# Optimization experiments

Measured on AMD Instinct MI355X. Metric: run time of the kernel, lower is better.

Reference implementation:

```python
import jax, jax.numpy as jnp
import numpy as np

HIDDEN = 128
N_HID = 7            # hidden_layers - 1 internal GELU blocks
N_TERMS = 2          # number of separable terms per side
N_IN = 1             # vars per term
B = 16384
STEP_SIZE = 0.1
NUM_STEPS = 1

# Forest-Ruth 4th-order symplectic coefficients
_K = 2.0 ** (1.0 / 3.0)
_C = (1.0 / (2.0 * (2.0 - _K)), (1.0 - _K) / (2.0 * (2.0 - _K)),
      (1.0 - _K) / (2.0 * (2.0 - _K)), 1.0 / (2.0 * (2.0 - _K)))
_D = (1.0 / (2.0 - _K), -_K / (2.0 - _K), 1.0 / (2.0 - _K), 0.0)


def _mlp(W0, b0, Wh, bh, Wo, bo, x):
    # x: [B, n_in] -> [B, 1]; torch GELU default is exact (erf)
    h = jax.nn.gelu(x @ W0 + b0, approximate=False)
    for i in range(N_HID):
        h = jax.nn.gelu(h @ Wh[i] + bh[i], approximate=False)
    return h @ Wo + bo


def _side_scalar(W0, b0, Wh, bh, Wo, bo, idx, x):
    # gather per-term feature subsets, run all term-MLPs batched via vmap,
    # sum over terms and batch (GradientWrapper takes grad of the summed scalar)
    xs = jnp.moveaxis(x[:, idx], 1, 0)            # [n_terms, B, n_in]
    outs = jax.vmap(_mlp)(W0, b0, Wh, bh, Wo, bo, xs)  # [n_terms, B, 1]
    return outs.sum()


def setup_inputs() -> dict:
    key = jax.random.key(0)
    ks = jax.random.split(key, 3)
    s = 0.05

    def pset(k):
        kk = jax.random.split(k, 6)
        return (
            jax.random.normal(kk[0], (N_TERMS, N_IN, HIDDEN), jnp.float32) * s,
            jax.random.normal(kk[1], (N_TERMS, HIDDEN), jnp.float32) * s,
            jax.random.normal(kk[2], (N_TERMS, N_HID, HIDDEN, HIDDEN), jnp.float32) * s,
            jax.random.normal(kk[3], (N_TERMS, N_HID, HIDDEN), jnp.float32) * s,
            jax.random.normal(kk[4], (N_TERMS, HIDDEN, 1), jnp.float32) * s,
            jax.random.normal(kk[5], (N_TERMS, 1), jnp.float32) * s,
        )

    lW0, lb0, lWh, lbh, lWo, lbo = pset(ks[0])
    rW0, rb0, rWh, rbh, rWo, rbo = pset(ks[1])
    X = jax.random.normal(ks[2], (B, 4), jnp.float32)
    left_idx = jnp.arange(N_TERMS, dtype=jnp.int32).reshape(N_TERMS, N_IN)
    right_idx = jnp.arange(N_TERMS, dtype=jnp.int32).reshape(N_TERMS, N_IN)
    return dict(X=X, lW0=lW0, lb0=lb0, lWh=lWh, lbh=lbh, lWo=lWo, lbo=lbo,
                rW0=rW0, rb0=rb0, rWh=rWh, rbh=rbh, rWo=rWo, rbo=rbo,
                left_idx=left_idx, right_idx=right_idx)


def reference(X, lW0, lb0, lWh, lbh, lWo, lbo,
              rW0, rb0, rWh, rbh, rWo, rbo, left_idx, right_idx):
    # H(q, p) = V(q) + T(p); left side = V(q), right side = T(p)
    dVdq = jax.grad(lambda q: _side_scalar(lW0, lb0, lWh, lbh, lWo, lbo, left_idx, q))
    dTdp = jax.grad(lambda p: _side_scalar(rW0, rb0, rWh, rbh, rWo, rbo, right_idx, p))
    dt = jnp.float32(STEP_SIZE)
    nq = X.shape[1] // 2
    q = X[:, :nq]
    p = X[:, nq:]
    for _ in range(NUM_STEPS):
        for c, d in zip(_C, _D):
            q = q + jnp.float32(c) * dt * dTdp(p)   # dq/dt =  dH/dp
            p = p - jnp.float32(d) * dt * dVdq(q)   # dp/dt = -dH/dq
    return jnp.concatenate((q, p), axis=1)
```

## Files before the change

### kernel.cpp

```cpp
#include <hip/hip_runtime.h>

#define NLAYER 7
#define IMGB 16384
#define WSCALE 16.0f

typedef __attribute__((ext_vector_type(2))) float float2v;
typedef __attribute__((ext_vector_type(4))) float float4v;
typedef __attribute__((ext_vector_type(4))) unsigned int uint4v;
typedef __attribute__((ext_vector_type(4))) int int4v;
typedef __attribute__((ext_vector_type(8))) int int8v;
typedef unsigned long long u64;

__device__ __forceinline__ float2v pk_fma(float2v a, float2v b, float2v c){
  return __builtin_elementwise_fma(a, b, c);
}
__device__ __forceinline__ float2v lo2(float4v v){ return (float2v){v[0], v[1]}; }
__device__ __forceinline__ float2v hi2(float4v v){ return (float2v){v[2], v[3]}; }

__device__ __forceinline__ unsigned pk4fp8(float v0, float v1, float v2, float v3){
  int w = __builtin_amdgcn_cvt_pk_fp8_f32(v0, v1, 0, false);
  w = __builtin_amdgcn_cvt_pk_fp8_f32(v2, v3, w, true);
  return (unsigned)w;
}
template<bool HI>
__device__ __forceinline__ float2v up2(unsigned w){
  return __builtin_amdgcn_cvt_pk_f32_fp8((int)w, HI);
}
__device__ __forceinline__ float4v mfma128s(int8v a, int8v b, unsigned sc){
  return __builtin_amdgcn_mfma_scale_f32_16x16x128_f8f6f4(
      a, b, (float4v){0.f,0.f,0.f,0.f}, 0, 0, 0, (int)sc, 0, 0x7F7F7F7F);
}
__device__ __forceinline__ void act2(float2v z, float2v& P16, float2v& gp16){
  const float2v c1v  = {6.3830764862829235f, 6.3830764862829235f};
  const float2v c3v  = {-1.0638460810704874f, -1.0638460810704874f};
  const float2v c33v = {-3.1915382432114624f, -3.1915382432114624f};
  const float2v v8   = {8.f, 8.f};
  float2v z2 = z * z;
  float2v u  = pk_fma(z2, c3v, c1v);
  P16 = pk_fma(z, u, v8);
  float2v Pd = pk_fma(z2, c33v, c1v);
  gp16 = pk_fma(z, Pd, P16);
}

__device__ __forceinline__ void gl2lds16(const unsigned char* g, unsigned char* l){
  __builtin_amdgcn_global_load_lds((const __attribute__((address_space(1))) unsigned int*)g,
                                   (__attribute__((address_space(3))) unsigned int*)l,
                                   16, 0, 0);
}

__device__ __forceinline__ int8v ld_op16(const unsigned char* lp, const unsigned char* hp){
  int4v lo = *(const int4v*)(lp);
  int4v hi = *(const int4v*)(hp);
  return __builtin_shufflevector(lo, hi, 0, 1, 2, 3, 4, 5, 6, 7);
}

__global__ __launch_bounds__(256)
void prep_weights(const float* __restrict__ lWh,
                  const float* __restrict__ rWh,
                  unsigned char* __restrict__ wbf)
{
  __shared__ __align__(16) unsigned char T[IMGB];
  const int b = blockIdx.x;
  const int net = b / NLAYER, L = b % NLAYER;
  const int side = net >> 1, term = net & 1;
  const float* src = (side ? rWh : lWh) + (size_t)((term*NLAYER + L)*128)*128;
  const int t = threadIdx.x;
  {
    const int k = t >> 1, n0 = (t & 1)*64;
    const float* row = src + k*128 + n0;
    #pragma unroll
    for (int c4 = 0; c4 < 4; ++c4){
      float4v f0 = *(const float4v*)(row + c4*16);
      float4v f1 = *(const float4v*)(row + c4*16 + 4);
      float4v f2 = *(const float4v*)(row + c4*16 + 8);
      float4v f3 = *(const float4v*)(row + c4*16 + 12);
      uint4v wv = { pk4fp8(f0[0]*WSCALE, f0[1]*WSCALE, f0[2]*WSCALE, f0[3]*WSCALE),
                    pk4fp8(f1[0]*WSCALE, f1[1]*WSCALE, f1[2]*WSCALE, f1[3]*WSCALE),
                    pk4fp8(f2[0]*WSCALE, f2[1]*WSCALE, f2[2]*WSCALE, f2[3]*WSCALE),
                    pk4fp8(f3[0]*WSCALE, f3[1]*WSCALE, f3[2]*WSCALE, f3[3]*WSCALE) };
      *(uint4v*)&T[k*128 + n0 + c4*16] = wv;
    }
  }
  __syncthreads();
  {
    const int n = t >> 1, c0 = (t & 1)*8;
    const int sw7 = n & 7;
    unsigned char* dst = wbf + ((size_t)b << 14) + n*128;
    #pragma unroll
    for (int c = 0; c < 8; ++c){
      const int c64 = c0 + c;
      const int kc = c64*8;
      u64 v = 0;
      #pragma unroll
      for (int j = 0; j < 8; ++j)
        v |= (u64)T[(kc + j)*128 + n] << (8*j);
      *(u64*)(dst + (((c64 >> 1) ^ sw7)*16) + (c64 & 1)*8) = v;
    }
  }
}

__global__ __launch_bounds__(512)
__attribute__((amdgpu_waves_per_eu(4, 4)))
void sympl_main(const float* __restrict__ X,
                const float* __restrict__ lW0, const float* __restrict__ lb0,
                const float* __restrict__ lbh, const float* __restrict__ lWo,
                const float* __restrict__ rW0, const float* __restrict__ rb0,
                const float* __restrict__ rbh, const float* __restrict__ rWo,
                const int* __restrict__ lidx, const int* __restrict__ ridx,
                const unsigned char* __restrict__ wbf,
                float* __restrict__ out)
{
  __shared__ __align__(16) unsigned char sWb[2*IMGB];
  __shared__ __align__(16) unsigned char sH[2*16384];

  const int tid  = threadIdx.x;
  const int lane = tid & 63;
  const int w    = tid >> 6;
  const int m0   = lane & 15;
  const int q    = lane >> 4;
  const int g2   = w & 3;
  const int ih   = w >> 2;
  const int col  = blockIdx.y;
  const int e0   = blockIdx.x * 64;
  const int r    = tid >> 3;
  const int sg   = tid & 7;
  const int r7   = r & 7;
  const int m06  = m0 & 6;
  const int m07  = m0 & 7;

  const int lt = (lidx[0] == col) ? 0 : 1;
  const int rt = (ridx[0] == col) ? 0 : 1;

  float qv = X[(e0 + r)*4 + col];
  float pv = X[(e0 + r)*4 + 2 + col];

  const float dt = 0.1f;
  const float C0 = 0.6756035959798289f, C1 = -0.17560359597982883f;
  const float D0 = 1.3512071919596578f, D1 = -1.7024143839193153f;
  const float is = 1.0f / 262144.0f;
  const float coefs[7] = { C0*dt*is, -D0*dt*is, C1*dt*is, -D1*dt*is,
                           C1*dt*is, -D0*dt*is, C0*dt*is };

  const int lo16 = (m0 & 1) * 16;
  const int opo  = ((2*q) ^ m06) * 16;
  const unsigned char* pB0lo = sH + (g2*16 + m0)*128 + opo + lo16;
  const unsigned char* pB0hi = sH + (g2*16 + m0)*128 + opo + 16 - lo16;
  const unsigned char* pA0lo = sWb + (ih*64 + m0)*128 + opo + lo16;
  const unsigned char* pA0hi = sWb + (ih*64 + m0)*128 + opo + 16 - lo16;
  unsigned char* pHe = sH + (g2*16 + m0)*128;
  unsigned char* pL0 = sH + r*128 + ((sg ^ r7)*16);
  const unsigned char* pRd = sH + 16384 + 8192 + r*128 + ((sg ^ r7)*16);
  const int q4 = q * 4;
  unsigned char* pE0 = pHe + ((ih*4 + 0) ^ m07)*16 + q4;
  unsigned char* pE1 = pHe + ((ih*4 + 1) ^ m07)*16 + q4;
  unsigned char* pE2 = pHe + ((ih*4 + 2) ^ m07)*16 + q4;
  unsigned char* pE3 = pHe + ((ih*4 + 3) ^ m07)*16 + q4;

  {
    const unsigned char* src = wbf + (size_t)(2 + rt)*NLAYER*IMGB;
    #pragma unroll
    for (int it = 0; it < 2; ++it){
      int o = (it*512 + tid) * 16;
      gl2lds16(src + o, sWb + o);
    }
  }
  __syncthreads();

  for (int ev = 0; ev < 7; ++ev){
    const bool isT = !(ev & 1);
    const int  evp = ev & 1;
    const int  term = isT ? rt : lt;
    const float* W0p = (isT ? rW0 : lW0) + term*128;
    const float* b0p = (isT ? rb0 : lb0) + term*128;
    const float* bhp = (isT ? rbh : lbh) + term*NLAYER*128;
    const float* Wop = (isT ? rWo : lWo) + term*128;
    const unsigned char* wimg = wbf + (size_t)(((isT ? 2 : 0) + term)*NLAYER)*IMGB;
    const int tnx = (ev & 1) ? rt : lt;
    const unsigned char* wimg_nx = wbf + (size_t)((((ev & 1) ? 2 : 0) + tnx)*NLAYER)*IMGB;

    float4v woa = *(const float4v*)(Wop + sg*16);
    float4v wob = *(const float4v*)(Wop + sg*16 + 4);
    float4v woc = *(const float4v*)(Wop + sg*16 + 8);
    float4v wod = *(const float4v*)(Wop + sg*16 + 12);

    {
      const float x = isT ? pv : qv;
      const float2v xv = {x, x};
      unsigned hw[4], dw[4];
      #pragma unroll
      for (int c = 0; c < 2; ++c){
        int n0 = sg*16 + c*8;
        float4v wa = *(const float4v*)(W0p + n0);
        float4v wb = *(const float4v*)(W0p + n0 + 4);
        float4v ba = *(const float4v*)(b0p + n0);
        float4v bb2 = *(const float4v*)(b0p + n0 + 4);
        float2v zp[4] = { pk_fma(xv, lo2(wa), lo2(ba)), pk_fma(xv, hi2(wa), hi2(ba)),
                          pk_fma(xv, lo2(wb), lo2(bb2)), pk_fma(xv, hi2(wb), hi2(bb2)) };
        float2v wp[4] = { lo2(wa), hi2(wa), lo2(wb), hi2(wb) };
        float Sh[8], Sd[8];
        #pragma unroll
        for (int pp = 0; pp < 4; ++pp){
          float2v P16, gp16; act2(zp[pp], P16, gp16);
          float2v h = zp[pp] * P16;
          float2v d = gp16 * wp[pp];
          Sh[pp*2] = h[0]; Sh[pp*2+1] = h[1];
          Sd[pp*2] = d[0]; Sd[pp*2+1] = d[1];
        }
        hw[c*2]   = pk4fp8(Sh[0],Sh[1],Sh[2],Sh[3]);
        hw[c*2+1] = pk4fp8(Sh[4],Sh[5],Sh[6],Sh[7]);
        dw[c*2]   = pk4fp8(Sd[0],Sd[1],Sd[2],Sd[3]);
        dw[c*2+1] = pk4fp8(Sd[4],Sd[5],Sd[6],Sd[7]);
      }
      *(uint4v*)(pL0)        = (uint4v){hw[0], hw[1], hw[2], hw[3]};
      *(uint4v*)(pL0 + 8192) = (uint4v){dw[0], dw[1], dw[2], dw[3]};
    }
    asm volatile("s_waitcnt lgkmcnt(0)" ::: "memory");
    __builtin_amdgcn_s_barrier();
    asm volatile("" ::: "memory");

    #pragma unroll
    for (int L = 0; L < NLAYER; ++L){
      const int rdo = (L & 1) * 16384;
      const int wro = rdo ^ 16384;
      const int par = (L & 1) ? (evp ^ 1) : evp;
      const int bufo = par ? IMGB : 0;
      const bool last = (L == NLAYER-1);

      const float* bias = bhp + L*128 + ih*64 + q4;
      float4v bv0 = *(const float4v*)(bias);
      float4v bv1 = *(const float4v*)(bias + 16);
      float4v bv2 = *(const float4v*)(bias + 32);
      float4v bv3 = *(const float4v*)(bias + 48);

      if (!(ev == 6 && L == 6)){
        const unsigned char* nsrc = (L < 6) ? (wimg + (size_t)(L+1)*IMGB) : wimg_nx;
        unsigned char* dW = sWb + (bufo ^ IMGB);
        #pragma unroll
        for (int it = 0; it < 2; ++it){
          int o = (it*512 + tid) * 16;
          gl2lds16(nsrc + o, dW + o);
        }
      }

      __builtin_amdgcn_s_setprio(1);
      const unsigned char* pAcLo = pA0lo + bufo;
      const unsigned char* pAcHi = pA0hi + bufo;
      int8v b0 = ld_op16(pB0lo + rdo, pB0hi + rdo);
      int8v b1 = ld_op16(pB0lo + rdo + 8192, pB0hi + rdo + 8192);
      float4v acc[4][2];
      #pragma unroll
      for (int i = 0; i < 4; ++i){
        int8v a = ld_op16(pAcLo + i*2048, pAcHi + i*2048);
        acc[i][0] = mfma128s(a, b0, 0x77777777u);
        acc[i][1] = mfma128s(a, b1, 0x79797979u);
      }
      __builtin_amdgcn_s_setprio(0);

      #define EPI(i, bvv, pe) { \
        float2v za = lo2(acc[i][0]) + lo2(bvv); \
        float2v zb = hi2(acc[i][0]) + hi2(bvv); \
        float2v ta = lo2(acc[i][1]); \
        float2v tb = hi2(acc[i][1]); \
        float2v Pa, ga, Pb, gb; \
        act2(za, Pa, ga); \
        act2(zb, Pb, gb); \
        float2v da = ga * ta, db = gb * tb; \
        if (!last){ \
          float2v ha = za * Pa, hb = zb * Pb; \
          *(unsigned*)(pe + wro) = pk4fp8(ha[0], ha[1], hb[0], hb[1]); \
        } \
        *(unsigned*)(pe + wro + 8192) = pk4fp8(da[0], da[1], db[0], db[1]); \
      }
      EPI(0, bv0, pE0)
      EPI(1, bv1, pE1)
      EPI(2, bv2, pE2)
      EPI(3, bv3, pE3)
      #undef EPI

      asm volatile("s_waitcnt vmcnt(0) lgkmcnt(0)" ::: "memory");
      __builtin_amdgcn_s_barrier();
      asm volatile("" ::: "memory");
    }

    {
      uint4v dvv = *(const uint4v*)(pRd);
      float2v sv = {0.f, 0.f};
      sv = pk_fma(up2<false>(dvv[0]), lo2(woa), sv);
      sv = pk_fma(up2<true>(dvv[0]),  hi2(woa), sv);
      sv = pk_fma(up2<false>(dvv[1]), lo2(wob), sv);
      sv = pk_fma(up2<true>(dvv[1]),  hi2(wob), sv);
      sv = pk_fma(up2<false>(dvv[2]), lo2(woc), sv);
      sv = pk_fma(up2<true>(dvv[2]),  hi2(woc), sv);
      sv = pk_fma(up2<false>(dvv[3]), lo2(wod), sv);
      sv = pk_fma(up2<true>(dvv[3]),  hi2(wod), sv);
      float s = sv[0] + sv[1];
      s += __shfl_xor(s, 1);
      s += __shfl_xor(s, 2);
      s += __shfl_xor(s, 4);
      if (isT) qv += coefs[ev] * s;
      else     pv += coefs[ev] * s;
    }
  }

  if (sg == 0){
    out[(e0 + r)*4 + col]     = qv;
    out[(e0 + r)*4 + 2 + col] = pv;
  }
}

extern "C" void kernel_launch(void* const* d_in, const int* in_sizes, int n_in,
                              void* d_out, int out_size, void* d_ws, size_t ws_size,
                              hipStream_t stream)
{
  const float* X   = (const float*)d_in[0];
  const float* lW0 = (const float*)d_in[1];
  const float* lb0 = (const float*)d_in[2];
  const float* lWh = (const float*)d_in[3];
  const float* lbh = (const float*)d_in[4];
  const float* lWo = (const float*)d_in[5];
  const float* rW0 = (const float*)d_in[7];
  const float* rb0 = (const float*)d_in[8];
  const float* rWh = (const float*)d_in[9];
  const float* rbh = (const float*)d_in[10];
  const float* rWo = (const float*)d_in[11];
  const int*   li  = (const int*)d_in[13];
  const int*   ri  = (const int*)d_in[14];
  unsigned char* wbf = (unsigned char*)d_ws;
  float* out = (float*)d_out;
  const int B = in_sizes[0] / 4;

  hipLaunchKernelGGL(prep_weights, dim3(4*NLAYER), dim3(256), 0, stream,
                     lWh, rWh, wbf);
  hipLaunchKernelGGL(sympl_main, dim3(B/64, 2), dim3(512), 0, stream,
                     X, lW0, lb0, lbh, lWo, rW0, rb0, rbh, rWo, li, ri, wbf, out);
}
```

Measured before the change: 180.8 us.

## Process both separable term columns in one block with doubled LDS buffers

```diff
diff --git a/kernel.cpp b/kernel.cpp
--- a/kernel.cpp
+++ b/kernel.cpp
@@ -3,6 +3,7 @@
 #define NLAYER 7
 #define IMGB 16384
 #define WSCALE 16.0f
+#define CH 32768
 
 typedef __attribute__((ext_vector_type(2))) float float2v;
 typedef __attribute__((ext_vector_type(4))) float float4v;
@@ -100,7 +101,7 @@
 }
 
 __global__ __launch_bounds__(512)
-__attribute__((amdgpu_waves_per_eu(4, 4)))
+__attribute__((amdgpu_waves_per_eu(2, 2)))
 void sympl_main(const float* __restrict__ X,
                 const float* __restrict__ lW0, const float* __restrict__ lb0,
                 const float* __restrict__ lbh, const float* __restrict__ lWo,
@@ -110,8 +111,8 @@
                 const unsigned char* __restrict__ wbf,
                 float* __restrict__ out)
 {
-  __shared__ __align__(16) unsigned char sWb[2*IMGB];
-  __shared__ __align__(16) unsigned char sH[2*16384];
+  __shared__ __align__(16) unsigned char sWb[4*IMGB];
+  __shared__ __align__(16) unsigned char sH[4*16384];
 
   const int tid  = threadIdx.x;
   const int lane = tid & 63;
@@ -120,7 +121,6 @@
   const int q    = lane >> 4;
   const int g2   = w & 3;
   const int ih   = w >> 2;
-  const int col  = blockIdx.y;
   const int e0   = blockIdx.x * 64;
   const int r    = tid >> 3;
   const int sg   = tid & 7;
@@ -128,11 +128,14 @@
   const int m06  = m0 & 6;
   const int m07  = m0 & 7;
 
-  const int lt = (lidx[0] == col) ? 0 : 1;
-  const int rt = (ridx[0] == col) ? 0 : 1;
-
-  float qv = X[(e0 + r)*4 + col];
-  float pv = X[(e0 + r)*4 + 2 + col];
+  const int li0 = lidx[0], ri0 = ridx[0];
+  const int ltA = (li0 == 0) ? 0 : 1, ltB = (li0 == 1) ? 0 : 1;
+  const int rtA = (ri0 == 0) ? 0 : 1, rtB = (ri0 == 1) ? 0 : 1;
+
+  float qvA = X[(e0 + r)*4 + 0];
+  float pvA = X[(e0 + r)*4 + 2];
+  float qvB = X[(e0 + r)*4 + 1];
+  float pvB = X[(e0 + r)*4 + 3];
 
   const float dt = 0.1f;
   const float C0 = 0.6756035959798289f, C1 = -0.17560359597982883f;
@@ -157,11 +160,13 @@
   unsigned char* pE3 = pHe + ((ih*4 + 3) ^ m07)*16 + q4;
 
   {
-    const unsigned char* src = wbf + (size_t)(2 + rt)*NLAYER*IMGB;
+    const unsigned char* srcA = wbf + (size_t)(2 + rtA)*NLAYER*IMGB;
+    const unsigned char* srcB = wbf + (size_t)(2 + rtB)*NLAYER*IMGB;
     #pragma unroll
     for (int it = 0; it < 2; ++it){
       int o = (it*512 + tid) * 16;
-      gl2lds16(src + o, sWb + o);
+      gl2lds16(srcA + o, sWb + o);
+      gl2lds16(srcB + o, sWb + CH + o);
     }
   }
   __syncthreads();
@@ -169,51 +174,65 @@
   for (int ev = 0; ev < 7; ++ev){
     const bool isT = !(ev & 1);
     const int  evp = ev & 1;
-    const int  term = isT ? rt : lt;
-    const float* W0p = (isT ? rW0 : lW0) + term*128;
-    const float* b0p = (isT ? rb0 : lb0) + term*128;
-    const float* bhp = (isT ? rbh : lbh) + term*NLAYER*128;
-    const float* Wop = (isT ? rWo : lWo) + term*128;
-    const unsigned char* wimg = wbf + (size_t)(((isT ? 2 : 0) + term)*NLAYER)*IMGB;
-    const int tnx = (ev & 1) ? rt : lt;
-    const unsigned char* wimg_nx = wbf + (size_t)((((ev & 1) ? 2 : 0) + tnx)*NLAYER)*IMGB;
-
-    float4v woa = *(const float4v*)(Wop + sg*16);
-    float4v wob = *(const float4v*)(Wop + sg*16 + 4);
-    float4v woc = *(const float4v*)(Wop + sg*16 + 8);
-    float4v wod = *(const float4v*)(Wop + sg*16 + 12);
-
-    {
-      const float x = isT ? pv : qv;
-      const float2v xv = {x, x};
-      unsigned hw[4], dw[4];
-      #pragma unroll
-      for (int c = 0; c < 2; ++c){
-        int n0 = sg*16 + c*8;
-        float4v wa = *(const float4v*)(W0p + n0);
-        float4v wb = *(const float4v*)(W0p + n0 + 4);
-        float4v ba = *(const float4v*)(b0p + n0);
-        float4v bb2 = *(const float4v*)(b0p + n0 + 4);
-        float2v zp[4] = { pk_fma(xv, lo2(wa), lo2(ba)), pk_fma(xv, hi2(wa), hi2(ba)),
-                          pk_fma(xv, lo2(wb), lo2(bb2)), pk_fma(xv, hi2(wb), hi2(bb2)) };
-        float2v wp[4] = { lo2(wa), hi2(wa), lo2(wb), hi2(wb) };
-        float Sh[8], Sd[8];
-        #pragma unroll
-        for (int pp = 0; pp < 4; ++pp){
-          float2v P16, gp16; act2(zp[pp], P16, gp16);
-          float2v h = zp[pp] * P16;
-          float2v d = gp16 * wp[pp];
-          Sh[pp*2] = h[0]; Sh[pp*2+1] = h[1];
-          Sd[pp*2] = d[0]; Sd[pp*2+1] = d[1];
-        }
-        hw[c*2]   = pk4fp8(Sh[0],Sh[1],Sh[2],Sh[3]);
-        hw[c*2+1] = pk4fp8(Sh[4],Sh[5],Sh[6],Sh[7]);
-        dw[c*2]   = pk4fp8(Sd[0],Sd[1],Sd[2],Sd[3]);
-        dw[c*2+1] = pk4fp8(Sd[4],Sd[5],Sd[6],Sd[7]);
-      }
-      *(uint4v*)(pL0)        = (uint4v){hw[0], hw[1], hw[2], hw[3]};
-      *(uint4v*)(pL0 + 8192) = (uint4v){dw[0], dw[1], dw[2], dw[3]};
-    }
+    const int  tA = isT ? rtA : ltA;
+    const int  tB = isT ? rtB : ltB;
+    const float* W0pA = (isT ? rW0 : lW0) + tA*128;
+    const float* b0pA = (isT ? rb0 : lb0) + tA*128;
+    const float* bhpA = (isT ? rbh : lbh) + tA*NLAYER*128;
+    const float* WopA = (isT ? rWo : lWo) + tA*128;
+    const float* W0pB = (isT ? rW0 : lW0) + tB*128;
+    const float* b0pB = (isT ? rb0 : lb0) + tB*128;
+    const float* bhpB = (isT ? rbh : lbh) + tB*NLAYER*128;
+    const float* WopB = (isT ? rWo : lWo) + tB*128;
+    const unsigned char* wimgA = wbf + (size_t)(((isT ? 2 : 0) + tA)*NLAYER)*IMGB;
+    const unsigned char* wimgB = wbf + (size_t)(((isT ? 2 : 0) + tB)*NLAYER)*IMGB;
+    const int tnxA = (ev & 1) ? rtA : ltA;
+    const int tnxB = (ev & 1) ? rtB : ltB;
+    const unsigned char* wimg_nxA = wbf + (size_t)((((ev & 1) ? 2 : 0) + tnxA)*NLAYER)*IMGB;
+    const unsigned char* wimg_nxB = wbf + (size_t)((((ev & 1) ? 2 : 0) + tnxB)*NLAYER)*IMGB;
+
+    float4v woaA = *(const float4v*)(WopA + sg*16);
+    float4v wobA = *(const float4v*)(WopA + sg*16 + 4);
+    float4v wocA = *(const float4v*)(WopA + sg*16 + 8);
+    float4v wodA = *(const float4v*)(WopA + sg*16 + 12);
+    float4v woaB = *(const float4v*)(WopB + sg*16);
+    float4v wobB = *(const float4v*)(WopB + sg*16 + 4);
+    float4v wocB = *(const float4v*)(WopB + sg*16 + 8);
+    float4v wodB = *(const float4v*)(WopB + sg*16 + 12);
+
+    #define LAYER0(xval, W0p, b0p, cho) { \
+      const float2v xv = {xval, xval}; \
+      unsigned hw[4], dw[4]; \
+      _Pragma("unroll") \
+      for (int c = 0; c < 2; ++c){ \
+        int n0 = sg*16 + c*8; \
+        float4v wa = *(const float4v*)(W0p + n0); \
+        float4v wb = *(const float4v*)(W0p + n0 + 4); \
+        float4v ba = *(const float4v*)(b0p + n0); \
+        float4v bb2 = *(const float4v*)(b0p + n0 + 4); \
+        float2v zp[4] = { pk_fma(xv, lo2(wa), lo2(ba)), pk_fma(xv, hi2(wa), hi2(ba)), \
+                          pk_fma(xv, lo2(wb), lo2(bb2)), pk_fma(xv, hi2(wb), hi2(bb2)) }; \
+        float2v wp[4] = { lo2(wa), hi2(wa), lo2(wb), hi2(wb) }; \
+        float Sh[8], Sd[8]; \
+        _Pragma("unroll") \
+        for (int pp = 0; pp < 4; ++pp){ \
+          float2v P16, gp16; act2(zp[pp], P16, gp16); \
+          float2v h = zp[pp] * P16; \
+          float2v d = gp16 * wp[pp]; \
+          Sh[pp*2] = h[0]; Sh[pp*2+1] = h[1]; \
+          Sd[pp*2] = d[0]; Sd[pp*2+1] = d[1]; \
+        } \
+        hw[c*2]   = pk4fp8(Sh[0],Sh[1],Sh[2],Sh[3]); \
+        hw[c*2+1] = pk4fp8(Sh[4],Sh[5],Sh[6],Sh[7]); \
+        dw[c*2]   = pk4fp8(Sd[0],Sd[1],Sd[2],Sd[3]); \
+        dw[c*2+1] = pk4fp8(Sd[4],Sd[5],Sd[6],Sd[7]); \
+      } \
+      *(uint4v*)(pL0 + cho)        = (uint4v){hw[0], hw[1], hw[2], hw[3]}; \
+      *(uint4v*)(pL0 + cho + 8192) = (uint4v){dw[0], dw[1], dw[2], dw[3]}; \
+    }
+    LAYER0((isT ? pvA : qvA), W0pA, b0pA, 0)
+    LAYER0((isT ? pvB : qvB), W0pB, b0pB, CH)
+    #undef LAYER0
     asm volatile("s_waitcnt lgkmcnt(0)" ::: "memory");
     __builtin_amdgcn_s_barrier();
     asm volatile("" ::: "memory");
@@ -226,37 +245,53 @@
       const int bufo = par ? IMGB : 0;
       const bool last = (L == NLAYER-1);
 
-      const float* bias = bhp + L*128 + ih*64 + q4;
-      float4v bv0 = *(const float4v*)(bias);
-      float4v bv1 = *(const float4v*)(bias + 16);
-      float4v bv2 = *(const float4v*)(bias + 32);
-      float4v bv3 = *(const float4v*)(bias + 48);
+      const float* biasA = bhpA + L*128 + ih*64 + q4;
+      float4v bvA0 = *(const float4v*)(biasA);
+      float4v bvA1 = *(const float4v*)(biasA + 16);
+      float4v bvA2 = *(const float4v*)(biasA + 32);
+      float4v bvA3 = *(const float4v*)(biasA + 48);
+      const float* biasB = bhpB + L*128 + ih*64 + q4;
+      float4v bvB0 = *(const float4v*)(biasB);
+      float4v bvB1 = *(const float4v*)(biasB + 16);
+      float4v bvB2 = *(const float4v*)(biasB + 32);
+      float4v bvB3 = *(const float4v*)(biasB + 48);
 
       if (!(ev == 6 && L == 6)){
-        const unsigned char* nsrc = (L < 6) ? (wimg + (size_t)(L+1)*IMGB) : wimg_nx;
-        unsigned char* dW = sWb + (bufo ^ IMGB);
+        const unsigned char* nsrcA = (L < 6) ? (wimgA + (size_t)(L+1)*IMGB) : wimg_nxA;
+        const unsigned char* nsrcB = (L < 6) ? (wimgB + (size_t)(L+1)*IMGB) : wimg_nxB;
+        unsigned char* dWA = sWb + (bufo ^ IMGB);
         #pragma unroll
         for (int it = 0; it < 2; ++it){
           int o = (it*512 + tid) * 16;
-          gl2lds16(nsrc + o, dW + o);
+          gl2lds16(nsrcA + o, dWA + o);
+          gl2lds16(nsrcB + o, dWA + CH + o);
         }
       }
 
       __builtin_amdgcn_s_setprio(1);
       const unsigned char* pAcLo = pA0lo + bufo;
       const unsigned char* pAcHi = pA0hi + bufo;
-      int8v b0 = ld_op16(pB0lo + rdo, pB0hi + rdo);
-      int8v b1 = ld_op16(pB0lo + rdo + 8192, pB0hi + rdo + 8192);
-      float4v acc[4][2];
+      int8v b0A = ld_op16(pB0lo + rdo, pB0hi + rdo);
+      int8v b1A = ld_op16(pB0lo + rdo + 8192, pB0hi + rdo + 8192);
+      float4v accA[4][2];
       #pragma unroll
       for (int i = 0; i < 4; ++i){
         int8v a = ld_op16(pAcLo + i*2048, pAcHi + i*2048);
-        acc[i][0] = mfma128s(a, b0, 0x77777777u);
-        acc[i][1] = mfma128s(a, b1, 0x79797979u);
+        accA[i][0] = mfma128s(a, b0A, 0x77777777u);
+        accA[i][1] = mfma128s(a, b1A, 0x79797979u);
+      }
+      int8v b0B = ld_op16(pB0lo + CH + rdo, pB0hi + CH + rdo);
+      int8v b1B = ld_op16(pB0lo + CH + rdo + 8192, pB0hi + CH + rdo + 8192);
+      float4v accB[4][2];
+      #pragma unroll
+      for (int i = 0; i < 4; ++i){
+        int8v a = ld_op16(pAcLo + CH + i*2048, pAcHi + CH + i*2048);
+        accB[i][0] = mfma128s(a, b0B, 0x77777777u);
+        accB[i][1] = mfma128s(a, b1B, 0x79797979u);
       }
       __builtin_amdgcn_s_setprio(0);
 
-      #define EPI(i, bvv, pe) { \
+      #define EPI(acc, i, bvv, pe, cho) { \
         float2v za = lo2(acc[i][0]) + lo2(bvv); \
         float2v zb = hi2(acc[i][0]) + hi2(bvv); \
         float2v ta = lo2(acc[i][1]); \
@@ -267,14 +302,18 @@
         float2v da = ga * ta, db = gb * tb; \
         if (!last){ \
           float2v ha = za * Pa, hb = zb * Pb; \
-          *(unsigned*)(pe + wro) = pk4fp8(ha[0], ha[1], hb[0], hb[1]); \
+          *(unsigned*)(pe + cho + wro) = pk4fp8(ha[0], ha[1], hb[0], hb[1]); \
         } \
-        *(unsigned*)(pe + wro + 8192) = pk4fp8(da[0], da[1], db[0], db[1]); \
+        *(unsigned*)(pe + cho + wro + 8192) = pk4fp8(da[0], da[1], db[0], db[1]); \
       }
-      EPI(0, bv0, pE0)
-      EPI(1, bv1, pE1)
-      EPI(2, bv2, pE2)
-      EPI(3, bv3, pE3)
+      EPI(accA, 0, bvA0, pE0, 0)
+      EPI(accA, 1, bvA1, pE1, 0)
+      EPI(accA, 2, bvA2, pE2, 0)
+      EPI(accA, 3, bvA3, pE3, 0)
+      EPI(accB, 0, bvB0, pE0, CH)
+      EPI(accB, 1, bvB1, pE1, CH)
+      EPI(accB, 2, bvB2, pE2, CH)
+      EPI(accB, 3, bvB3, pE3, CH)
       #undef EPI
 
       asm volatile("s_waitcnt vmcnt(0) lgkmcnt(0)" ::: "memory");
@@ -282,29 +321,34 @@
       asm volatile("" ::: "memory");
     }
 
-    {
-      uint4v dvv = *(const uint4v*)(pRd);
-      float2v sv = {0.f, 0.f};
-      sv = pk_fma(up2<false>(dvv[0]), lo2(woa), sv);
-      sv = pk_fma(up2<true>(dvv[0]),  hi2(woa), sv);
-      sv = pk_fma(up2<false>(dvv[1]), lo2(wob), sv);
-      sv = pk_fma(up2<true>(dvv[1]),  hi2(wob), sv);
-      sv = pk_fma(up2<false>(dvv[2]), lo2(woc), sv);
-      sv = pk_fma(up2<true>(dvv[2]),  hi2(woc), sv);
-      sv = pk_fma(up2<false>(dvv[3]), lo2(wod), sv);
-      sv = pk_fma(up2<true>(dvv[3]),  hi2(wod), sv);
-      float s = sv[0] + sv[1];
-      s += __shfl_xor(s, 1);
-      s += __shfl_xor(s, 2);
-      s += __shfl_xor(s, 4);
-      if (isT) qv += coefs[ev] * s;
-      else     pv += coefs[ev] * s;
-    }
+    #define REDUCE(cho, woa, wob, woc, wod, qvv, pvv) { \
+      uint4v dvv = *(const uint4v*)(pRd + cho); \
+      float2v sv = {0.f, 0.f}; \
+      sv = pk_fma(up2<false>(dvv[0]), lo2(woa), sv); \
+      sv = pk_fma(up2<true>(dvv[0]),  hi2(woa), sv); \
+      sv = pk_fma(up2<false>(dvv[1]), lo2(wob), sv); \
+      sv = pk_fma(up2<true>(dvv[1]),  hi2(wob), sv); \
+      sv = pk_fma(up2<false>(dvv[2]), lo2(woc), sv); \
+      sv = pk_fma(up2<true>(dvv[2]),  hi2(woc), sv); \
+      sv = pk_fma(up2<false>(dvv[3]), lo2(wod), sv); \
+      sv = pk_fma(up2<true>(dvv[3]),  hi2(wod), sv); \
+      float s = sv[0] + sv[1]; \
+      s += __shfl_xor(s, 1); \
+      s += __shfl_xor(s, 2); \
+      s += __shfl_xor(s, 4); \
+      if (isT) qvv += coefs[ev] * s; \
+      else     pvv += coefs[ev] * s; \
+    }
+    REDUCE(0,  woaA, wobA, wocA, wodA, qvA, pvA)
+    REDUCE(CH, woaB, wobB, wocB, wodB, qvB, pvB)
+    #undef REDUCE
   }
 
   if (sg == 0){
-    out[(e0 + r)*4 + col]     = qv;
-    out[(e0 + r)*4 + 2 + col] = pv;
+    out[(e0 + r)*4 + 0] = qvA;
+    out[(e0 + r)*4 + 2] = pvA;
+    out[(e0 + r)*4 + 1] = qvB;
+    out[(e0 + r)*4 + 3] = pvB;
   }
 }
 
@@ -331,6 +375,6 @@
 
   hipLaunchKernelGGL(prep_weights, dim3(4*NLAYER), dim3(256), 0, stream,
                      lWh, rWh, wbf);
-  hipLaunchKernelGGL(sympl_main, dim3(B/64, 2), dim3(512), 0, stream,
+  hipLaunchKernelGGL(sympl_main, dim3(B/64), dim3(512), 0, stream,
                      X, lW0, lb0, lbh, lWo, rW0, rb0, rbh, rWo, li, ri, wbf, out);
 }
```

After: 207.8 us. 14.9% more time.
